# Performance work log

Hardware: AMD Instinct MI355X
Metric: run time of the kernel (lower is better)

The kernel has to match this reference:

```python
import jax, jax.numpy as jnp
import numpy as np

N, E, D, T, R, H = 50000, 400000, 256, 3, 6, 4
DK = D // H          # 64, d_k = out_dim // n_heads
OUT = H * DK         # 256
LN_EPS = 1e-5


def setup_inputs() -> dict:
    key = jax.random.key(0)
    ks = jax.random.split(key, 16)
    std = 0.02  # initializer_range in HGTClassfication._init_weights
    f32 = jnp.float32
    inp = {
        "x": jax.random.normal(ks[0], (N, D), f32),
        "Wk": jax.random.normal(ks[1], (T, D, OUT), f32) * std,
        "bk": jnp.zeros((T, OUT), f32),
        "Wq": jax.random.normal(ks[2], (T, D, OUT), f32) * std,
        "bq": jnp.zeros((T, OUT), f32),
        "Wv": jax.random.normal(ks[3], (T, D, OUT), f32) * std,
        "bv": jnp.zeros((T, OUT), f32),
        "Wa": jax.random.normal(ks[4], (T, OUT, OUT), f32) * std,
        "ba": jnp.zeros((T, OUT), f32),
        "rel_pri": jnp.ones((R, H), f32),
        "rel_att": jax.random.normal(ks[5], (R, H, DK, DK), f32) * (1.0 / np.sqrt(DK)),
        "rel_msg": jax.random.normal(ks[6], (R, H, DK, DK), f32) * (1.0 / np.sqrt(DK)),
        "skip": jnp.ones((T,), f32),
        "ln_g": jnp.ones((T, OUT), f32),
        "ln_b": jnp.zeros((T, OUT), f32),
        "node_type": jax.random.randint(ks[7], (N,), 0, T),
        "edge_src": jax.random.randint(ks[8], (E,), 0, N),
        "edge_dst": jax.random.randint(ks[9], (E,), 0, N),
        "edge_type": jax.random.randint(ks[10], (E,), 0, R),
        "n_heads": H,
    }
    return inp


def reference(x, Wk, bk, Wq, bq, Wv, bv, Wa, ba, rel_pri, rel_att, rel_msg,
              skip, ln_g, ln_b, node_type, edge_src, edge_dst, edge_type, n_heads):
    n, d = x.shape
    r, h = rel_pri.shape
    dk = rel_att.shape[-1]
    out_dim = h * dk
    ar = jnp.arange(n)

    def typed_linear(inp_, W, b):
        # per-node-type Linear: compute for all T types, pick by node_type
        y = jnp.einsum('ni,tio->tno', inp_, W) + b[:, None, :]
        return y[node_type, ar]

    k = typed_linear(x, Wk, bk).reshape(n, h, dk)
    q = typed_linear(x, Wq, bq).reshape(n, h, dk)
    v = typed_linear(x, Wv, bv).reshape(n, h, dk)

    # relation-specific transforms (done on nodes, gathered per edge: N*R << E*R work)
    k_rel = jnp.einsum('nhd,rhde->rnhe', k, rel_att)   # [R,N,H,dk]
    v_rel = jnp.einsum('nhd,rhde->rnhe', v, rel_msg)   # [R,N,H,dk]
    key_e = k_rel[edge_type, edge_src]                 # [E,H,dk]
    val_e = v_rel[edge_type, edge_src]                 # [E,H,dk]

    att = (q[edge_dst] * key_e).sum(-1) * rel_pri[edge_type] / jnp.sqrt(jnp.float32(dk))  # [E,H]

    # per-(dst, etype) mailbox softmax + weighted sum (DGL reduce per canonical etype)
    seg = edge_dst * r + edge_type
    S = n * r
    amax = jax.ops.segment_max(att, seg, num_segments=S)
    amax = jax.lax.stop_gradient(jnp.where(jnp.isfinite(amax), amax, 0.0))
    ex = jnp.exp(att - amax[seg])
    denom = jax.ops.segment_sum(ex, seg, num_segments=S)
    w = ex / denom[seg]                                # [E,H]
    hsum = jax.ops.segment_sum(w[:, :, None] * val_e, seg, num_segments=S)  # [S,H,dk]
    cnt = jax.ops.segment_sum(jnp.ones((seg.shape[0],), x.dtype), seg, num_segments=S)

    # cross_reducer='mean' over relations that delivered messages
    t_rel = hsum.reshape(n, r, out_dim)
    present = cnt.reshape(n, r) > 0
    nrel = jnp.maximum(present.sum(-1), 1).astype(x.dtype)
    t = (t_rel * present[..., None].astype(x.dtype)).sum(1) / nrel[:, None]

    trans = typed_linear(t, Wa, ba)
    alpha = jax.nn.sigmoid(skip)[node_type][:, None]
    out = trans * alpha + x * (1.0 - alpha)

    mu = out.mean(-1, keepdims=True)
    var = out.var(-1, keepdims=True)
    normed = (out - mu) * jax.lax.rsqrt(var + LN_EPS) * ln_g[node_type] + ln_b[node_type]

    # nodes with no incoming edges keep their input feature (no 't' in DGL data)
    has_msg = present.any(-1)[:, None]
    return jnp.where(has_msg, normed, x)
```

## Files before the change

### kernel.cpp

```cpp
#include <hip/hip_runtime.h>
#include <hip/hip_bf16.h>


#define NN 50000
#define EE 400000
#define TN 3
#define RN 6
#define HN 4
#define SS (NN * RN)
#define NCHUNK 293
#define CD 16

typedef __hip_bfloat16 bf16;
typedef unsigned short u16;
using bf16x8 = __attribute__((ext_vector_type(8))) __bf16;
using f32x4  = __attribute__((ext_vector_type(4))) float;

__device__ __forceinline__ float b2f(bf16 h) { return __bfloat162float(h); }
__device__ __forceinline__ float busf(u16 u) { return __uint_as_float((unsigned)u << 16); }
__device__ __forceinline__ float blo(unsigned u) { return __uint_as_float(u << 16); }
__device__ __forceinline__ float bhi(unsigned u) { return __uint_as_float(u & 0xffff0000u); }
__device__ __forceinline__ u16 f2us(float f) {
    unsigned u = __float_as_uint(f);
    return (u16)((u + 0x7fffu + ((u >> 16) & 1u)) >> 16);
}
__device__ __forceinline__ float ld(const void* p, long i, int f) {
    return f ? ((const float*)p)[i] : b2f(((const bf16*)p)[i]);
}

__global__ __launch_bounds__(256) void detect_dtype(const void* __restrict__ x,
                                                    int* __restrict__ flag) {
    __shared__ int cnt_s;
    if (threadIdx.x == 0) cnt_s = 0;
    __syncthreads();
    const u16* p = (const u16*)x;
    int c = 0;
    for (int i = threadIdx.x; i < 8192; i += 256) {
        int expo = (p[i] >> 7) & 0xFF;
        if (expo >= 0x97) ++c;
    }
    atomicAdd(&cnt_s, c);
    __syncthreads();
    if (threadIdx.x == 0) *flag = (cnt_s > 64) ? 1 : 0;
}

__global__ __launch_bounds__(256) void prep(const void* __restrict__ rel_att,
        const void* __restrict__ rel_msg,
        const void* __restrict__ Wk, const void* __restrict__ Wq,
        const void* __restrict__ Wv, const void* __restrict__ Wa,
        const void* __restrict__ x, const int* __restrict__ node_type,
        const int* __restrict__ edst, const int* __restrict__ etype,
        const int* __restrict__ flag,
        u16* __restrict__ MTa, u16* __restrict__ MTm,
        u16* __restrict__ WallT, u16* __restrict__ WaT,
        u16* __restrict__ xb,
        int* __restrict__ lists, int* __restrict__ cnts,
        unsigned* __restrict__ cnt) {
    int b = blockIdx.x;
    int t = threadIdx.x;
    if (b < 48) {
        int f = *flag;
        int m = b;
        long base = (long)(m % 24) * 4096;
        if (m < 24) {
            for (int it = 0; it < 16; ++it) {
                int idx = it * 256 + t;
                MTa[base + idx] = f2us(ld(rel_att, base + idx, f));
            }
        } else {
            for (int it = 0; it < 16; ++it) {
                int idx = it * 256 + t;
                int d = idx >> 6, j = idx & 63;
                MTm[base + (j << 6) + d] = f2us(ld(rel_msg, base + idx, f));
            }
        }
    } else if (b < 3120) {
        int f = *flag;
        int m = b - 48;
        if (m < 2304) {
            int ty = m / 768, o3 = m % 768;
            int sec = o3 >> 8, o = o3 & 255;
            const void* W = (sec == 0) ? Wk : (sec == 1) ? Wq : Wv;
            WallT[(size_t)ty * 768 * 256 + (size_t)o3 * 256 + t] =
                f2us(ld(W, (long)ty * 65536 + (long)t * 256 + o, f));
        } else {
            int mm = m - 2304;
            int ty = mm / 256, o = mm % 256;
            WaT[(size_t)ty * 65536 + (size_t)o * 256 + t] =
                f2us(ld(Wa, (long)ty * 65536 + (long)t * 256 + o, f));
        }
    } else if (b < 15620) {
        int f = *flag;
        long i = ((long)(b - 3120) * 256 + t) * 4;
        if (i < (long)NN * 256) {
            if (f) {
                float4 v = *(const float4*)((const float*)x + i);
                ushort4 p; p.x = f2us(v.x); p.y = f2us(v.y); p.z = f2us(v.z); p.w = f2us(v.w);
                *(ushort4*)(xb + i) = p;
            } else {
                *(ushort4*)(xb + i) = *(const ushort4*)((const u16*)x + i);
            }
        }
    } else if (b < 15816) {
        __shared__ int lc[TN], lbase[TN];
        if (t < TN) lc[t] = 0;
        __syncthreads();
        int n = (b - 15620) * 256 + t;
        int pos = -1, ty = 0;
        if (n < NN) {
            ty = node_type[n];
            pos = atomicAdd(&lc[ty], 1);
        }
        __syncthreads();
        if (t < TN) lbase[t] = atomicAdd(&cnts[t], lc[t]);
        __syncthreads();
        if (n < NN) lists[ty * NN + lbase[ty] + pos] = n;
    } else {
        int e = (b - 15816) * 256 + t;
        if (e < EE) atomicAdd(&cnt[etype[e] * NN + edst[e]], 1u);
    }
}

__global__ __launch_bounds__(256) void scanA(const unsigned* __restrict__ cnt,
                                             unsigned* __restrict__ csums) {
    __shared__ unsigned s[256];
    int b = blockIdx.x, t = threadIdx.x;
    int s0 = b * 1024 + t * 4;
    unsigned v = 0;
    if (s0 + 3 < SS) { uint4 u = *(const uint4*)&cnt[s0]; v = u.x + u.y + u.z + u.w; }
    else { for (int j = 0; j < 4; ++j) if (s0 + j < SS) v += cnt[s0 + j]; }
    s[t] = v;
    __syncthreads();
    for (int st = 128; st > 0; st >>= 1) {
        if (t < st) s[t] += s[t + st];
        __syncthreads();
    }
    if (t == 0) csums[b] = s[0];
}

__global__ __launch_bounds__(256) void scanB(unsigned* __restrict__ csums,
                                             int* __restrict__ base) {
    __shared__ unsigned s[512];
    int t = threadIdx.x;
    unsigned a = (t < NCHUNK) ? csums[t] : 0u;
    unsigned b = (256 + t < NCHUNK) ? csums[256 + t] : 0u;
    s[t] = a; s[256 + t] = b;
    __syncthreads();
    for (int st = 1; st < 512; st <<= 1) {
        unsigned x0 = (t >= st) ? s[t - st] : 0u;
        unsigned x1 = (256 + t >= st) ? s[256 + t - st] : 0u;
        __syncthreads();
        s[t] += x0; s[256 + t] += x1;
        __syncthreads();
    }
    if (t < NCHUNK) csums[t] = s[t] - a;
    if (256 + t < NCHUNK) csums[256 + t] = s[256 + t] - b;
    if (t == 0) base[SS] = (int)s[NCHUNK - 1];
}

__global__ __launch_bounds__(256) void scanC(const unsigned* __restrict__ cnt,
        const unsigned* __restrict__ csums, int* __restrict__ base) {
    __shared__ unsigned s[256];
    int b = blockIdx.x, t = threadIdx.x;
    int s0 = b * 1024 + t * 4;
    unsigned vs[4] = {0u, 0u, 0u, 0u};
    if (s0 + 3 < SS) { uint4 u = *(const uint4*)&cnt[s0]; vs[0]=u.x; vs[1]=u.y; vs[2]=u.z; vs[3]=u.w; }
    else { for (int j = 0; j < 4; ++j) if (s0 + j < SS) vs[j] = cnt[s0 + j]; }
    unsigned v = vs[0] + vs[1] + vs[2] + vs[3];
    s[t] = v;
    __syncthreads();
    for (int st = 1; st < 256; st <<= 1) {
        unsigned x = (t >= st) ? s[t - st] : 0u;
        __syncthreads();
        s[t] += x;
        __syncthreads();
    }
    unsigned run = csums[b] + s[t] - v;
    for (int j = 0; j < 4; ++j) {
        if (s0 + j < SS) { base[s0 + j] = (int)run; run += vs[j]; }
    }
}

__global__ __launch_bounds__(256) void scatter_edges(const int* __restrict__ edst,
        const int* __restrict__ etype, const int* __restrict__ base,
        unsigned* __restrict__ cnt, int* __restrict__ sorted) {
    int e = blockIdx.x * 256 + threadIdx.x;
    if (e >= EE) return;
    int seg = etype[e] * NN + edst[e];
    unsigned old = atomicSub(&cnt[seg], 1u);
    sorted[base[seg] + (int)old - 1] = e;
}

__global__ __launch_bounds__(512, 2) void k1_mfma(const u16* __restrict__ xb,
        const u16* __restrict__ WallT,
        const void* __restrict__ bk, const void* __restrict__ bq,
        const void* __restrict__ bv,
        const int* __restrict__ lists, const int* __restrict__ cnts,
        const int* __restrict__ flag,
        u16* __restrict__ kb, u16* __restrict__ qb, u16* __restrict__ vb) {
    int f = *flag;
    int tt = blockIdx.x % TN, tile = blockIdx.x / TN;
    int cnt = cnts[tt];
    int start = tile * 64;
    if (start >= cnt) return;
    __shared__ int nl[64];
    __shared__ __align__(16) u16 xs[64][280];
    __shared__ __align__(16) float bias_s[768];
    int t = threadIdx.x;
    if (t < 64) nl[t] = (start + t < cnt) ? lists[tt * NN + start + t] : -1;
    if (t < 256) {
        bias_s[t]       = ld(bk, tt * 256 + t, f);
        bias_s[256 + t] = ld(bq, tt * 256 + t, f);
        bias_s[512 + t] = ld(bv, tt * 256 + t, f);
    }
    __syncthreads();
    {
        int i = t >> 4, g = t & 15;
        #pragma unroll
        for (int i2 = 0; i2 < 2; ++i2) {
            int row = i + i2 * 32;
            int node = nl[row];
            uint4 a = {0, 0, 0, 0}, b = {0, 0, 0, 0};
            if (node >= 0) {
                const uint4* src = (const uint4*)(xb + (size_t)node * 256 + g * 16);
                a = src[0]; b = src[1];
            }
            *(uint4*)&xs[row][g * 16] = a;
            *(uint4*)&xs[row][g * 16 + 8] = b;
        }
    }
    __syncthreads();
    int w = t >> 6, lane = t & 63, ln = lane & 15, quad = lane >> 4;
    const u16* Wt = WallT + (size_t)tt * 768 * 256;
    f32x4 acc[6][4];
    #pragma unroll
    for (int j = 0; j < 6; ++j)
        #pragma unroll
        for (int g = 0; g < 4; ++g)
            acc[j][g] = (f32x4){0.f, 0.f, 0.f, 0.f};
    for (int kt = 0; kt < 8; ++kt) {
        bf16x8 A[6];
        #pragma unroll
        for (int jt = 0; jt < 6; ++jt)
            A[jt] = *(const bf16x8*)(Wt + (size_t)(w * 96 + jt * 16 + ln) * 256 + kt * 32 + quad * 8);
        bf16x8 B[4];
        #pragma unroll
        for (int g = 0; g < 4; ++g)
            B[g] = *(const bf16x8*)&xs[g * 16 + ln][kt * 32 + quad * 8];
        #pragma unroll
        for (int jt = 0; jt < 6; ++jt)
            #pragma unroll
            for (int g = 0; g < 4; ++g)
                acc[jt][g] = __builtin_amdgcn_mfma_f32_16x16x32_bf16(A[jt], B[g], acc[jt][g], 0, 0, 0);
    }
    #pragma unroll
    for (int jt = 0; jt < 6; ++jt) {
        int jc = w * 96 + jt * 16 + quad * 4;
        float4 bi = *(const float4*)&bias_s[jc];
        int sec = jc >> 8, o = jc & 255;
        u16* basep = (sec == 0 ? kb : sec == 1 ? qb : vb);
        #pragma unroll
        for (int g = 0; g < 4; ++g) {
            int node = nl[g * 16 + ln];
            if (node >= 0) {
                ushort4 p;
                p.x = f2us(acc[jt][g][0] + bi.x); p.y = f2us(acc[jt][g][1] + bi.y);
                p.z = f2us(acc[jt][g][2] + bi.z); p.w = f2us(acc[jt][g][3] + bi.w);
                *(ushort4*)(basep + (size_t)node * 256 + o) = p;
            }
        }
    }
}

__global__ __launch_bounds__(256) void k2k4(const u16* __restrict__ kb,
        const u16* __restrict__ qb, const u16* __restrict__ vb,
        const u16* __restrict__ MTa, const u16* __restrict__ MTm,
        const void* __restrict__ rel_pri,
        const int* __restrict__ sorted, const int* __restrict__ base,
        const int* __restrict__ esrc,
        const int* __restrict__ flag, float* __restrict__ tacc) {
    int f = *flag;
    int c0 = blockIdx.x * CD;
    int nd = min(CD, NN - c0);
    __shared__ int sb_[CD + 1];
    __shared__ __align__(16) u16 qL[CD][264];
    __shared__ __align__(16) u16 qrelL[CD][264];
    __shared__ __align__(16) u16 srawL[CD][264];
    int t = threadIdx.x;
    int w = t >> 6, lane = t & 63, ln = lane & 15, quad = lane >> 4;
    int half = lane >> 5, lane32 = lane & 31;
    int hh = lane32 >> 3;
    {
        int i = t >> 4, g = t & 15;
        uint4 a0 = {0,0,0,0}, a1 = {0,0,0,0};
        if (i < nd) {
            const uint4* src = (const uint4*)(qb + (size_t)(c0 + i) * 256 + g * 16);
            a0 = src[0]; a1 = src[1];
        }
        *(uint4*)&qL[i][g * 16] = a0;
        *(uint4*)&qL[i][g * 16 + 8] = a1;
    }
    f32x4 accF[4];
    #pragma unroll
    for (int m = 0; m < 4; ++m) accF[m] = (f32x4){0.f, 0.f, 0.f, 0.f};

    for (int r = 0; r < RN; ++r) {
        if (t <= nd) sb_[t] = base[r * NN + c0 + t];
        __syncthreads();
        long mtbase = (long)(r * HN + w) * 4096;
        {
            bf16x8 B0 = *(const bf16x8*)&qL[ln][w * 64 + quad * 8];
            bf16x8 B1 = *(const bf16x8*)&qL[ln][w * 64 + quad * 8 + 32];
            #pragma unroll
            for (int mt = 0; mt < 4; ++mt) {
                const u16* ap = MTa + mtbase + (mt * 16 + ln) * 64 + quad * 8;
                bf16x8 A0 = *(const bf16x8*)(ap);
                bf16x8 A1 = *(const bf16x8*)(ap + 32);
                f32x4 acc = {0.f, 0.f, 0.f, 0.f};
                acc = __builtin_amdgcn_mfma_f32_16x16x32_bf16(A0, B0, acc, 0, 0, 0);
                acc = __builtin_amdgcn_mfma_f32_16x16x32_bf16(A1, B1, acc, 0, 0, 0);
                int jc = w * 64 + mt * 16 + quad * 4;
                ushort4 pq;
                pq.x = f2us(acc[0]); pq.y = f2us(acc[1]);
                pq.z = f2us(acc[2]); pq.w = f2us(acc[3]);
                *(ushort4*)&qrelL[ln][jc] = pq;
            }
        }
        __syncthreads();
        {
            float pri = ld(rel_pri, r * HN + hh, f) * 0.125f;
            for (int i2 = w * 2 + half; i2 < nd; i2 += 8) {
                int sb = sb_[i2], se = sb_[i2 + 1];
                float a0=0.f,a1=0.f,a2=0.f,a3=0.f,a4=0.f,a5=0.f,a6=0.f,a7=0.f;
                if (se > sb) {
                    uint4 qv = *(const uint4*)&qrelL[i2][lane32 * 8];
                    float q0=blo(qv.x),q1=bhi(qv.x),q2=blo(qv.y),q3=bhi(qv.y);
                    float q4=blo(qv.z),q5=bhi(qv.z),q6=blo(qv.w),q7=bhi(qv.w);
                    float den = 0.f;
                    for (int idx = sb; idx < se; ++idx) {
                        int e = sorted[idx];
                        int s = esrc[e];
                        size_t rowoff = (size_t)s * 256 + lane32 * 8;
                        uint4 kv = *(const uint4*)(kb + rowoff);
                        uint4 vv = *(const uint4*)(vb + rowoff);
                        float d = blo(kv.x)*q0 + bhi(kv.x)*q1 + blo(kv.y)*q2 + bhi(kv.y)*q3
                                + blo(kv.z)*q4 + bhi(kv.z)*q5 + blo(kv.w)*q6 + bhi(kv.w)*q7;
                        d += __shfl_xor(d, 1); d += __shfl_xor(d, 2); d += __shfl_xor(d, 4);
                        float attv = fminf(fmaxf(d * pri, -50.f), 50.f);
                        float ex = expf(attv);
                        den += ex;
                        a0 += ex * blo(vv.x); a1 += ex * bhi(vv.x);
                        a2 += ex * blo(vv.y); a3 += ex * bhi(vv.y);
                        a4 += ex * blo(vv.z); a5 += ex * bhi(vv.z);
                        a6 += ex * blo(vv.w); a7 += ex * bhi(vv.w);
                    }
                    float inv = 1.f / den;
                    a0 *= inv; a1 *= inv; a2 *= inv; a3 *= inv;
                    a4 *= inv; a5 *= inv; a6 *= inv; a7 *= inv;
                }
                u16 pv8[8];
                pv8[0]=f2us(a0); pv8[1]=f2us(a1); pv8[2]=f2us(a2); pv8[3]=f2us(a3);
                pv8[4]=f2us(a4); pv8[5]=f2us(a5); pv8[6]=f2us(a6); pv8[7]=f2us(a7);
                *(uint4*)&srawL[i2][lane32 * 8] = *(const uint4*)pv8;
            }
        }
        __syncthreads();
        {
            bf16x8 B0 = *(const bf16x8*)&srawL[ln][w * 64 + quad * 8];
            bf16x8 B1 = *(const bf16x8*)&srawL[ln][w * 64 + quad * 8 + 32];
            #pragma unroll
            for (int mt = 0; mt < 4; ++mt) {
                const u16* mp = MTm + mtbase + (mt * 16 + ln) * 64 + quad * 8;
                bf16x8 A0 = *(const bf16x8*)(mp);
                bf16x8 A1 = *(const bf16x8*)(mp + 32);
                accF[mt] = __builtin_amdgcn_mfma_f32_16x16x32_bf16(A0, B0, accF[mt], 0, 0, 0);
                accF[mt] = __builtin_amdgcn_mfma_f32_16x16x32_bf16(A1, B1, accF[mt], 0, 0, 0);
            }
        }
    }
    if (ln < nd) {
        #pragma unroll
        for (int mt = 0; mt < 4; ++mt) {
            int jc = w * 64 + mt * 16 + quad * 4;
            float4 v = {accF[mt][0], accF[mt][1], accF[mt][2], accF[mt][3]};
            *(float4*)(tacc + (long)(c0 + ln) * 256 + jc) = v;
        }
    }
}

__global__ __launch_bounds__(512, 4) void k5_fused(const void* __restrict__ x,
        const float* __restrict__ tacc, const u16* __restrict__ WaT,
        const void* __restrict__ ba, const void* __restrict__ skip,
        const void* __restrict__ ln_g, const void* __restrict__ ln_b,
        const int* __restrict__ base,
        const int* __restrict__ lists, const int* __restrict__ cnts,
        const int* __restrict__ flag, void* out) {
    int f = *flag;
    int tt = blockIdx.x % TN, tile = blockIdx.x / TN;
    int cnt = cnts[tt];
    int start = tile * 64;
    if (start >= cnt) return;
    __shared__ int nl[64];
    __shared__ float invs[64];
    __shared__ int hasv[64];
    __shared__ __align__(16) u16 xs[64][280];
    __shared__ __align__(16) float ba_s[256], lnG_s[256], lnB_s[256];
    __shared__ float red1[64][8], red2[64][8];
    __shared__ float mu_[64], rs_[64];
    int t = threadIdx.x;
    if (t < 64) {
        int node = (start + t < cnt) ? lists[tt * NN + start + t] : -1;
        nl[t] = node;
        int nrel = 0;
        if (node >= 0) {
            #pragma unroll
            for (int r = 0; r < RN; ++r)
                nrel += (base[r * NN + node + 1] > base[r * NN + node]) ? 1 : 0;
        }
        hasv[t] = nrel;
        invs[t] = (nrel > 0) ? 1.f / (float)nrel : 1.f;
    }
    if (t < 256) {
        ba_s[t]  = ld(ba,   tt * 256 + t, f);
        lnG_s[t] = ld(ln_g, tt * 256 + t, f);
        lnB_s[t] = ld(ln_b, tt * 256 + t, f);
    }
    __syncthreads();
    {
        int i = t >> 3, g8 = t & 7;
        int node = nl[i];
        float inv = invs[i];
        int o0 = g8 * 32;
        u16 tmp[32];
        if (node >= 0) {
            const float* src = tacc + (long)node * 256 + o0;
            #pragma unroll
            for (int j = 0; j < 8; ++j) {
                float4 v = *(const float4*)(src + j * 4);
                tmp[j*4+0] = f2us(v.x * inv); tmp[j*4+1] = f2us(v.y * inv);
                tmp[j*4+2] = f2us(v.z * inv); tmp[j*4+3] = f2us(v.w * inv);
            }
        } else {
            #pragma unroll
            for (int j = 0; j < 32; ++j) tmp[j] = 0;
        }
        #pragma unroll
        for (int j = 0; j < 4; ++j)
            *(uint4*)&xs[i][o0 + j * 8] = ((const uint4*)tmp)[j];
    }
    __syncthreads();
    int w = t >> 6, lane = t & 63, ln = lane & 15, quad = lane >> 4;
    const u16* Wt = WaT + (size_t)tt * 65536;
    f32x4 acc[2][4];
    #pragma unroll
    for (int j = 0; j < 2; ++j)
        #pragma unroll
        for (int g = 0; g < 4; ++g)
            acc[j][g] = (f32x4){0.f, 0.f, 0.f, 0.f};
    for (int kt = 0; kt < 8; ++kt) {
        bf16x8 A[2];
        #pragma unroll
        for (int jt = 0; jt < 2; ++jt)
            A[jt] = *(const bf16x8*)(Wt + (size_t)(w * 32 + jt * 16 + ln) * 256 + kt * 32 + quad * 8);
        bf16x8 B[4];
        #pragma unroll
        for (int g = 0; g < 4; ++g)
            B[g] = *(const bf16x8*)&xs[g * 16 + ln][kt * 32 + quad * 8];
        #pragma unroll
        for (int jt = 0; jt < 2; ++jt)
            #pragma unroll
            for (int g = 0; g < 4; ++g)
                acc[jt][g] = __builtin_amdgcn_mfma_f32_16x16x32_bf16(A[jt], B[g], acc[jt][g], 0, 0, 0);
    }
    float sk = ld(skip, tt, f);
    float alpha = 1.f / (1.f + expf(-sk));
    float p1[4] = {0.f, 0.f, 0.f, 0.f}, p2[4] = {0.f, 0.f, 0.f, 0.f};
    #pragma unroll
    for (int g = 0; g < 4; ++g) {
        int node = nl[g * 16 + ln];
        if (node < 0) continue;
        #pragma unroll
        for (int jt = 0; jt < 2; ++jt) {
            int jc = w * 32 + jt * 16 + quad * 4;
            float4 bi = *(const float4*)&ba_s[jc];
            long xo = (long)node * 256 + jc;
            float xv[4];
            if (f) {
                float4 v = *(const float4*)((const float*)x + xo);
                xv[0] = v.x; xv[1] = v.y; xv[2] = v.z; xv[3] = v.w;
            } else {
                ushort4 v = *(const ushort4*)((const u16*)x + xo);
                xv[0] = busf(v.x); xv[1] = busf(v.y); xv[2] = busf(v.z); xv[3] = busf(v.w);
            }
            #pragma unroll
            for (int rg = 0; rg < 4; ++rg) {
                float ov = acc[jt][g][rg] + ((const float*)&bi)[rg];
                ov = ov * alpha + xv[rg] * (1.f - alpha);
                acc[jt][g][rg] = ov;
                p1[g] += ov; p2[g] += ov * ov;
            }
        }
    }
    #pragma unroll
    for (int g = 0; g < 4; ++g) {
        p1[g] += __shfl_xor(p1[g], 16); p1[g] += __shfl_xor(p1[g], 32);
        p2[g] += __shfl_xor(p2[g], 16); p2[g] += __shfl_xor(p2[g], 32);
    }
    if (quad == 0) {
        #pragma unroll
        for (int g = 0; g < 4; ++g) {
            red1[g * 16 + ln][w] = p1[g];
            red2[g * 16 + ln][w] = p2[g];
        }
    }
    __syncthreads();
    if (t < 64) {
        float s1 = 0.f, s2 = 0.f;
        #pragma unroll
        for (int j = 0; j < 8; ++j) { s1 += red1[t][j]; s2 += red2[t][j]; }
        float mu = s1 * (1.f / 256.f);
        float ms = s2 * (1.f / 256.f);
        float var = fmaxf(ms - mu * mu, 0.f);
        mu_[t] = mu; rs_[t] = rsqrtf(var + 1e-5f);
    }
    __syncthreads();
    #pragma unroll
    for (int g = 0; g < 4; ++g) {
        int li = g * 16 + ln;
        int node = nl[li];
        if (node < 0) continue;
        if (hasv[li] > 0) {
            float mu = mu_[li], rs = rs_[li];
            #pragma unroll
            for (int jt = 0; jt < 2; ++jt) {
                int jc = w * 32 + jt * 16 + quad * 4;
                float4 gg = *(const float4*)&lnG_s[jc];
                float4 bb = *(const float4*)&lnB_s[jc];
                long oo = (long)node * 256 + jc;
                float r0 = (acc[jt][g][0] - mu) * rs * gg.x + bb.x;
                float r1 = (acc[jt][g][1] - mu) * rs * gg.y + bb.y;
                float r2 = (acc[jt][g][2] - mu) * rs * gg.z + bb.z;
                float r3 = (acc[jt][g][3] - mu) * rs * gg.w + bb.w;
                if (f) { float4 v = {r0, r1, r2, r3}; *(float4*)((float*)out + oo) = v; }
                else   { ushort4 v; v.x = f2us(r0); v.y = f2us(r1); v.z = f2us(r2); v.w = f2us(r3);
                         *(ushort4*)((u16*)out + oo) = v; }
            }
        } else {
            #pragma unroll
            for (int jt = 0; jt < 2; ++jt) {
                int jc = w * 32 + jt * 16 + quad * 4;
                long oo = (long)node * 256 + jc;
                if (f) { *(float4*)((float*)out + oo) = *(const float4*)((const float*)x + oo); }
                else   { *(ushort4*)((u16*)out + oo) = *(const ushort4*)((const u16*)x + oo); }
            }
        }
    }
}

extern "C" void kernel_launch(void* const* d_in, const int* in_sizes, int n_in,
                              void* d_out, int out_size, void* d_ws, size_t ws_size,
                              hipStream_t stream) {
    const void* x       = d_in[0];
    const void* Wk      = d_in[1];
    const void* bk      = d_in[2];
    const void* Wq      = d_in[3];
    const void* bq      = d_in[4];
    const void* Wv      = d_in[5];
    const void* bv      = d_in[6];
    const void* Wa      = d_in[7];
    const void* ba      = d_in[8];
    const void* rel_pri = d_in[9];
    const void* rel_att = d_in[10];
    const void* rel_msg = d_in[11];
    const void* skip    = d_in[12];
    const void* ln_g    = d_in[13];
    const void* ln_b    = d_in[14];
    const int* node_type = (const int*)d_in[15];
    const int* edge_src  = (const int*)d_in[16];
    const int* edge_dst  = (const int*)d_in[17];
    const int* edge_type = (const int*)d_in[18];
    char* w = (char*)d_ws;

    u16*      kb     = (u16*)(w);
    u16*      qb     = (u16*)(w + 25600000);
    u16*      vb     = (u16*)(w + 51200000);
    float*    tacc   = (float*)(w + 76800000);
    u16*      xb     = (u16*)(w + 76800000);
    u16*      attex  = (u16*)(w + 128000000);
    int*      sorted = (int*)(w + 131200000);
    int*      base   = (int*)(w + 132800000);
    int*      nlists = (int*)(w + 134000064);
    u16*      MTa    = (u16*)(w + 134600064);
    u16*      MTm    = (u16*)(w + 134796672);
    u16*      WallT  = (u16*)(w + 134993280);
    u16*      WaT    = (u16*)(w + 136172928);
    unsigned* cnt    = (unsigned*)(w + 136566144);
    int*      ncnts  = (int*)(w + 137766144);
    int*      flag   = (int*)(w + 137766208);
    unsigned* csums  = (unsigned*)(w + 137766272);
    (void)attex;

    hipMemsetAsync(w + 136566144, 0, 1201408, stream);

    detect_dtype<<<dim3(1), dim3(256), 0, stream>>>(x, flag);
    prep<<<dim3(17379), dim3(256), 0, stream>>>(
        rel_att, rel_msg, Wk, Wq, Wv, Wa, x, node_type, edge_dst, edge_type,
        flag, MTa, MTm, WallT, WaT, xb, nlists, ncnts, cnt);
    scanA<<<dim3(NCHUNK), dim3(256), 0, stream>>>(cnt, csums);
    scanB<<<dim3(1), dim3(256), 0, stream>>>(csums, base);
    scanC<<<dim3(NCHUNK), dim3(256), 0, stream>>>(cnt, csums, base);
    scatter_edges<<<dim3((EE + 255) / 256), dim3(256), 0, stream>>>(
        edge_dst, edge_type, base, cnt, sorted);

    k1_mfma<<<dim3(TN * ((NN + 63) / 64)), dim3(512), 0, stream>>>(
        xb, WallT, bk, bq, bv, nlists, ncnts, flag, kb, qb, vb);


    k2k4<<<dim3(NN / CD), dim3(256), 0, stream>>>(
        kb, qb, vb, MTa, MTm, rel_pri, sorted, base, edge_src,
        flag, tacc);

    k5_fused<<<dim3(TN * ((NN + 63) / 64)), dim3(512), 0, stream>>>(
        x, tacc, WaT, ba, skip, ln_g, ln_b, base, nlists, ncnts, flag, d_out);
}
```

Before: 591.6 us.

## Store edge sources in sorted list and interleave two segments per gather loop

```diff
diff --git a/kernel.cpp b/kernel.cpp
--- a/kernel.cpp
+++ b/kernel.cpp
@@ -182,13 +182,14 @@
 }
 
 __global__ __launch_bounds__(256) void scatter_edges(const int* __restrict__ edst,
-        const int* __restrict__ etype, const int* __restrict__ base,
+        const int* __restrict__ etype, const int* __restrict__ esrc,
+        const int* __restrict__ base,
         unsigned* __restrict__ cnt, int* __restrict__ sorted) {
     int e = blockIdx.x * 256 + threadIdx.x;
     if (e >= EE) return;
     int seg = etype[e] * NN + edst[e];
     unsigned old = atomicSub(&cnt[seg], 1u);
-    sorted[base[seg] + (int)old - 1] = e;
+    sorted[base[seg] + (int)old - 1] = esrc[e];
 }
 
 __global__ __launch_bounds__(512, 2) void k1_mfma(const u16* __restrict__ xb,
@@ -277,12 +278,11 @@
         const u16* __restrict__ MTa, const u16* __restrict__ MTm,
         const void* __restrict__ rel_pri,
         const int* __restrict__ sorted, const int* __restrict__ base,
-        const int* __restrict__ esrc,
         const int* __restrict__ flag, float* __restrict__ tacc) {
     int f = *flag;
     int c0 = blockIdx.x * CD;
     int nd = min(CD, NN - c0);
-    __shared__ int sb_[CD + 1];
+    __shared__ int sb2_[RN][CD + 1];
     __shared__ __align__(16) u16 qL[CD][264];
     __shared__ __align__(16) u16 qrelL[CD][264];
     __shared__ __align__(16) u16 srawL[CD][264];
@@ -290,6 +290,10 @@
     int w = t >> 6, lane = t & 63, ln = lane & 15, quad = lane >> 4;
     int half = lane >> 5, lane32 = lane & 31;
     int hh = lane32 >> 3;
+    if (t < RN * (CD + 1)) {
+        int rr = t / (CD + 1), ii = t % (CD + 1);
+        sb2_[rr][ii] = base[rr * NN + c0 + ii];
+    }
     {
         int i = t >> 4, g = t & 15;
         uint4 a0 = {0,0,0,0}, a1 = {0,0,0,0};
@@ -303,69 +307,97 @@
     f32x4 accF[4];
     #pragma unroll
     for (int m = 0; m < 4; ++m) accF[m] = (f32x4){0.f, 0.f, 0.f, 0.f};
+    __syncthreads();
+    {
+        long mtbase = 0L * HN * 4096 + (long)w * 4096;
+        bf16x8 B0 = *(const bf16x8*)&qL[ln][w * 64 + quad * 8];
+        bf16x8 B1 = *(const bf16x8*)&qL[ln][w * 64 + quad * 8 + 32];
+        #pragma unroll
+        for (int mt = 0; mt < 4; ++mt) {
+            const u16* ap = MTa + mtbase + (mt * 16 + ln) * 64 + quad * 8;
+            bf16x8 A0 = *(const bf16x8*)(ap);
+            bf16x8 A1 = *(const bf16x8*)(ap + 32);
+            f32x4 acc = {0.f, 0.f, 0.f, 0.f};
+            acc = __builtin_amdgcn_mfma_f32_16x16x32_bf16(A0, B0, acc, 0, 0, 0);
+            acc = __builtin_amdgcn_mfma_f32_16x16x32_bf16(A1, B1, acc, 0, 0, 0);
+            int jc = w * 64 + mt * 16 + quad * 4;
+            ushort4 pq;
+            pq.x = f2us(acc[0]); pq.y = f2us(acc[1]);
+            pq.z = f2us(acc[2]); pq.w = f2us(acc[3]);
+            *(ushort4*)&qrelL[ln][jc] = pq;
+        }
+    }
+    __syncthreads();
 
     for (int r = 0; r < RN; ++r) {
-        if (t <= nd) sb_[t] = base[r * NN + c0 + t];
-        __syncthreads();
-        long mtbase = (long)(r * HN + w) * 4096;
-        {
-            bf16x8 B0 = *(const bf16x8*)&qL[ln][w * 64 + quad * 8];
-            bf16x8 B1 = *(const bf16x8*)&qL[ln][w * 64 + quad * 8 + 32];
-            #pragma unroll
-            for (int mt = 0; mt < 4; ++mt) {
-                const u16* ap = MTa + mtbase + (mt * 16 + ln) * 64 + quad * 8;
-                bf16x8 A0 = *(const bf16x8*)(ap);
-                bf16x8 A1 = *(const bf16x8*)(ap + 32);
-                f32x4 acc = {0.f, 0.f, 0.f, 0.f};
-                acc = __builtin_amdgcn_mfma_f32_16x16x32_bf16(A0, B0, acc, 0, 0, 0);
-                acc = __builtin_amdgcn_mfma_f32_16x16x32_bf16(A1, B1, acc, 0, 0, 0);
-                int jc = w * 64 + mt * 16 + quad * 4;
-                ushort4 pq;
-                pq.x = f2us(acc[0]); pq.y = f2us(acc[1]);
-                pq.z = f2us(acc[2]); pq.w = f2us(acc[3]);
-                *(ushort4*)&qrelL[ln][jc] = pq;
-            }
-        }
-        __syncthreads();
         {
             float pri = ld(rel_pri, r * HN + hh, f) * 0.125f;
-            for (int i2 = w * 2 + half; i2 < nd; i2 += 8) {
-                int sb = sb_[i2], se = sb_[i2 + 1];
-                float a0=0.f,a1=0.f,a2=0.f,a3=0.f,a4=0.f,a5=0.f,a6=0.f,a7=0.f;
-                if (se > sb) {
-                    uint4 qv = *(const uint4*)&qrelL[i2][lane32 * 8];
-                    float q0=blo(qv.x),q1=bhi(qv.x),q2=blo(qv.y),q3=bhi(qv.y);
-                    float q4=blo(qv.z),q5=bhi(qv.z),q6=blo(qv.w),q7=bhi(qv.w);
-                    float den = 0.f;
-                    for (int idx = sb; idx < se; ++idx) {
-                        int e = sorted[idx];
-                        int s = esrc[e];
-                        size_t rowoff = (size_t)s * 256 + lane32 * 8;
-                        uint4 kv = *(const uint4*)(kb + rowoff);
-                        uint4 vv = *(const uint4*)(vb + rowoff);
-                        float d = blo(kv.x)*q0 + bhi(kv.x)*q1 + blo(kv.y)*q2 + bhi(kv.y)*q3
-                                + blo(kv.z)*q4 + bhi(kv.z)*q5 + blo(kv.w)*q6 + bhi(kv.w)*q7;
-                        d += __shfl_xor(d, 1); d += __shfl_xor(d, 2); d += __shfl_xor(d, 4);
-                        float attv = fminf(fmaxf(d * pri, -50.f), 50.f);
-                        float ex = expf(attv);
-                        den += ex;
-                        a0 += ex * blo(vv.x); a1 += ex * bhi(vv.x);
-                        a2 += ex * blo(vv.y); a3 += ex * bhi(vv.y);
-                        a4 += ex * blo(vv.z); a5 += ex * bhi(vv.z);
-                        a6 += ex * blo(vv.w); a7 += ex * bhi(vv.w);
-                    }
-                    float inv = 1.f / den;
-                    a0 *= inv; a1 *= inv; a2 *= inv; a3 *= inv;
-                    a4 *= inv; a5 *= inv; a6 *= inv; a7 *= inv;
+            int iA = w * 2 + half;
+            int iB = iA + 8;
+            int sbA = sb2_[r][iA], nA = sb2_[r][iA + 1] - sbA;
+            int sbB = sb2_[r][iB], nB = sb2_[r][iB + 1] - sbB;
+            float aA0=0.f,aA1=0.f,aA2=0.f,aA3=0.f,aA4=0.f,aA5=0.f,aA6=0.f,aA7=0.f;
+            float aB0=0.f,aB1=0.f,aB2=0.f,aB3=0.f,aB4=0.f,aB5=0.f,aB6=0.f,aB7=0.f;
+            float denA = 0.f, denB = 0.f;
+            uint4 qvA = *(const uint4*)&qrelL[iA][lane32 * 8];
+            uint4 qvB = *(const uint4*)&qrelL[iB][lane32 * 8];
+            int nmax = max(nA, nB);
+            for (int j = 0; j < nmax; ++j) {
+                uint4 kvA, vvA, kvB, vvB;
+                bool doA = (j < nA), doB = (j < nB);
+                int sA = doA ? sorted[sbA + j] : 0;
+                int sB = doB ? sorted[sbB + j] : 0;
+                size_t roA = (size_t)sA * 256 + lane32 * 8;
+                size_t roB = (size_t)sB * 256 + lane32 * 8;
+                if (doA) { kvA = *(const uint4*)(kb + roA); vvA = *(const uint4*)(vb + roA); }
+                if (doB) { kvB = *(const uint4*)(kb + roB); vvB = *(const uint4*)(vb + roB); }
+                if (doA) {
+                    float d = blo(kvA.x)*blo(qvA.x) + bhi(kvA.x)*bhi(qvA.x)
+                            + blo(kvA.y)*blo(qvA.y) + bhi(kvA.y)*bhi(qvA.y)
+                            + blo(kvA.z)*blo(qvA.z) + bhi(kvA.z)*bhi(qvA.z)
+                            + blo(kvA.w)*blo(qvA.w) + bhi(kvA.w)*bhi(qvA.w);
+                    d += __shfl_xor(d, 1); d += __shfl_xor(d, 2); d += __shfl_xor(d, 4);
+                    float attv = fminf(fmaxf(d * pri, -50.f), 50.f);
+                    float ex = expf(attv);
+                    denA += ex;
+                    aA0 += ex * blo(vvA.x); aA1 += ex * bhi(vvA.x);
+                    aA2 += ex * blo(vvA.y); aA3 += ex * bhi(vvA.y);
+                    aA4 += ex * blo(vvA.z); aA5 += ex * bhi(vvA.z);
+                    aA6 += ex * blo(vvA.w); aA7 += ex * bhi(vvA.w);
                 }
+                if (doB) {
+                    float d = blo(kvB.x)*blo(qvB.x) + bhi(kvB.x)*bhi(qvB.x)
+                            + blo(kvB.y)*blo(qvB.y) + bhi(kvB.y)*bhi(qvB.y)
+                            + blo(kvB.z)*blo(qvB.z) + bhi(kvB.z)*bhi(qvB.z)
+                            + blo(kvB.w)*blo(qvB.w) + bhi(kvB.w)*bhi(qvB.w);
+                    d += __shfl_xor(d, 1); d += __shfl_xor(d, 2); d += __shfl_xor(d, 4);
+                    float attv = fminf(fmaxf(d * pri, -50.f), 50.f);
+                    float ex = expf(attv);
+                    denB += ex;
+                    aB0 += ex * blo(vvB.x); aB1 += ex * bhi(vvB.x);
+                    aB2 += ex * blo(vvB.y); aB3 += ex * bhi(vvB.y);
+                    aB4 += ex * blo(vvB.z); aB5 += ex * bhi(vvB.z);
+                    aB6 += ex * blo(vvB.w); aB7 += ex * bhi(vvB.w);
+                }
+            }
+            {
+                float inv = (nA > 0) ? 1.f / denA : 0.f;
                 u16 pv8[8];
-                pv8[0]=f2us(a0); pv8[1]=f2us(a1); pv8[2]=f2us(a2); pv8[3]=f2us(a3);
-                pv8[4]=f2us(a4); pv8[5]=f2us(a5); pv8[6]=f2us(a6); pv8[7]=f2us(a7);
-                *(uint4*)&srawL[i2][lane32 * 8] = *(const uint4*)pv8;
+                pv8[0]=f2us(aA0*inv); pv8[1]=f2us(aA1*inv); pv8[2]=f2us(aA2*inv); pv8[3]=f2us(aA3*inv);
+                pv8[4]=f2us(aA4*inv); pv8[5]=f2us(aA5*inv); pv8[6]=f2us(aA6*inv); pv8[7]=f2us(aA7*inv);
+                *(uint4*)&srawL[iA][lane32 * 8] = *(const uint4*)pv8;
+            }
+            {
+                float inv = (nB > 0) ? 1.f / denB : 0.f;
+                u16 pv8[8];
+                pv8[0]=f2us(aB0*inv); pv8[1]=f2us(aB1*inv); pv8[2]=f2us(aB2*inv); pv8[3]=f2us(aB3*inv);
+                pv8[4]=f2us(aB4*inv); pv8[5]=f2us(aB5*inv); pv8[6]=f2us(aB6*inv); pv8[7]=f2us(aB7*inv);
+                *(uint4*)&srawL[iB][lane32 * 8] = *(const uint4*)pv8;
             }
         }
         __syncthreads();
         {
+            long mtbase = (long)(r * HN + w) * 4096;
             bf16x8 B0 = *(const bf16x8*)&srawL[ln][w * 64 + quad * 8];
             bf16x8 B1 = *(const bf16x8*)&srawL[ln][w * 64 + quad * 8 + 32];
             #pragma unroll
@@ -376,7 +408,27 @@
                 accF[mt] = __builtin_amdgcn_mfma_f32_16x16x32_bf16(A0, B0, accF[mt], 0, 0, 0);
                 accF[mt] = __builtin_amdgcn_mfma_f32_16x16x32_bf16(A1, B1, accF[mt], 0, 0, 0);
             }
-        }
+            if (r + 1 < RN) {
+                long mtbase2 = (long)((r + 1) * HN + w) * 4096;
+                bf16x8 Q0 = *(const bf16x8*)&qL[ln][w * 64 + quad * 8];
+                bf16x8 Q1 = *(const bf16x8*)&qL[ln][w * 64 + quad * 8 + 32];
+                #pragma unroll
+                for (int mt = 0; mt < 4; ++mt) {
+                    const u16* ap = MTa + mtbase2 + (mt * 16 + ln) * 64 + quad * 8;
+                    bf16x8 A0 = *(const bf16x8*)(ap);
+                    bf16x8 A1 = *(const bf16x8*)(ap + 32);
+                    f32x4 acc = {0.f, 0.f, 0.f, 0.f};
+                    acc = __builtin_amdgcn_mfma_f32_16x16x32_bf16(A0, Q0, acc, 0, 0, 0);
+                    acc = __builtin_amdgcn_mfma_f32_16x16x32_bf16(A1, Q1, acc, 0, 0, 0);
+                    int jc = w * 64 + mt * 16 + quad * 4;
+                    ushort4 pq;
+                    pq.x = f2us(acc[0]); pq.y = f2us(acc[1]);
+                    pq.z = f2us(acc[2]); pq.w = f2us(acc[3]);
+                    *(ushort4*)&qrelL[ln][jc] = pq;
+                }
+            }
+        }
+        __syncthreads();
     }
     if (ln < nd) {
         #pragma unroll
@@ -610,15 +662,14 @@
     scanB<<<dim3(1), dim3(256), 0, stream>>>(csums, base);
     scanC<<<dim3(NCHUNK), dim3(256), 0, stream>>>(cnt, csums, base);
     scatter_edges<<<dim3((EE + 255) / 256), dim3(256), 0, stream>>>(
-        edge_dst, edge_type, base, cnt, sorted);
+        edge_dst, edge_type, edge_src, base, cnt, sorted);
 
     k1_mfma<<<dim3(TN * ((NN + 63) / 64)), dim3(512), 0, stream>>>(
         xb, WallT, bk, bq, bv, nlists, ncnts, flag, kb, qb, vb);
 
 
     k2k4<<<dim3(NN / CD), dim3(256), 0, stream>>>(
-        kb, qb, vb, MTa, MTm, rel_pri, sorted, base, edge_src,
-        flag, tacc);
+        kb, qb, vb, MTa, MTm, rel_pri, sorted, base, flag, tacc);
 
     k5_fused<<<dim3(TN * ((NN + 63) / 64)), dim3(512), 0, stream>>>(
         x, tacc, WaT, ba, skip, ln_g, ln_b, base, nlists, ncnts, flag, d_out);
```

Measured after the change: 553.9 us. 1.07x faster.
